# Performance work log

Hardware: AMD Instinct MI355X
Metric: run time of the kernel (lower is better)

The kernel has to match this reference:

```python
import jax, jax.numpy as jnp
import numpy as np

N = 50000      # nodes
E = 500000     # edges
D = 128        # model dim (in_dim == out_dim)
H = 8          # heads
DH = D // H    # head dim = 16
BN_EPS = 1e-5
Z_EPS = 1e-6


def setup_inputs() -> dict:
    key = jax.random.key(0)
    ks = jax.random.split(key, 24)
    w = lambda k, shape, s=0.05: (jax.random.normal(k, shape, jnp.float32) * s)
    inp = {}
    inp['v'] = jax.random.normal(ks[0], (N, D), jnp.float32)
    inp['e'] = jax.random.normal(ks[1], (E, D), jnp.float32)
    inp['envelope'] = jax.random.uniform(ks[2], (E, 1, 1), jnp.float32)
    inp['src'] = jax.random.randint(ks[3], (E,), 0, N, jnp.int32)
    inp['dst'] = jax.random.randint(ks[4], (E,), 0, N, jnp.int32)
    # attention projections (use_bias=False)
    inp['WQ'] = w(ks[5], (D, D)); inp['WK'] = w(ks[6], (D, D))
    inp['WV'] = w(ks[7], (D, D)); inp['We'] = w(ks[8], (D, D))
    # output projections
    inp['WO_v'] = w(ks[9], (D, D)); inp['bO_v'] = jnp.zeros((D,), jnp.float32)
    inp['WO_e'] = w(ks[10], (D, D)); inp['bO_e'] = jnp.zeros((D,), jnp.float32)
    # batch-norm affine params
    inp['g1_v'] = jnp.ones((D,), jnp.float32); inp['b1_v'] = jnp.zeros((D,), jnp.float32)
    inp['g1_e'] = jnp.ones((D,), jnp.float32); inp['b1_e'] = jnp.zeros((D,), jnp.float32)
    inp['g2_v'] = jnp.ones((D,), jnp.float32); inp['b2_v'] = jnp.zeros((D,), jnp.float32)
    inp['g2_e'] = jnp.ones((D,), jnp.float32); inp['b2_e'] = jnp.zeros((D,), jnp.float32)
    # FFN weights (hidden = 2*D)
    inp['W1v'] = w(ks[11], (D, 2 * D)); inp['b1v'] = jnp.zeros((2 * D,), jnp.float32)
    inp['W2v'] = w(ks[12], (2 * D, D)); inp['b2v'] = jnp.zeros((D,), jnp.float32)
    inp['W1e'] = w(ks[13], (D, 2 * D)); inp['b1e'] = jnp.zeros((2 * D,), jnp.float32)
    inp['W2e'] = w(ks[14], (2 * D, D)); inp['b2e'] = jnp.zeros((D,), jnp.float32)
    return inp


def _batchnorm(x, g, b):
    # BatchNorm1d in training mode: biased batch stats over axis 0
    m = x.mean(0)
    var = x.var(0)
    return (x - m) * jax.lax.rsqrt(var + BN_EPS) * g + b


def _forward(v, e, envelope, src, dst,
             WQ, WK, WV, We, WO_v, bO_v, WO_e, bO_e,
             g1_v, b1_v, g1_e, b1_e,
             W1v, b1v, W2v, b2v, W1e, b1e, W2e, b2e,
             g2_v, b2_v, g2_e, b2_e):
    # --- multi-head edge attention ---
    Q = (v @ WQ).reshape(N, H, DH)
    K = (v @ WK).reshape(N, H, DH)
    V = (v @ WV).reshape(N, H, DH)
    pe = (e @ We).reshape(E, H, DH)
    # score = K[src] * Q[dst] / sqrt(Dh) * proj_e   (elementwise, per head)
    score = K[src] * Q[dst] / np.sqrt(DH).astype(np.float32) * pe  # [E,H,Dh]
    e_attn = score.reshape(E, D)                                    # e_out
    s = jnp.exp(jnp.clip(score.sum(-1, keepdims=True), -5.0, 5.0))  # [E,H,1]
    msg = V[src] * envelope * s                                     # [E,H,Dh]
    wV = jax.ops.segment_sum(msg, dst, num_segments=N)              # [N,H,Dh]
    z = jax.ops.segment_sum(s, dst, num_segments=N)                 # [N,H,1]
    v_attn = (wV / (z + Z_EPS)).reshape(N, D)
    # --- O projection + residual + batchnorm ---
    v1 = _batchnorm(v + (v_attn @ WO_v + bO_v), g1_v, b1_v)
    e1 = _batchnorm(e + (e_attn @ WO_e + bO_e), g1_e, b1_e)
    # --- FFN + residual + batchnorm ---
    v2 = _batchnorm(v1 + (jax.nn.relu(v1 @ W1v + b1v) @ W2v + b2v), g2_v, b2_v)
    e2 = _batchnorm(e1 + (jax.nn.relu(e1 @ W1e + b1e) @ W2e + b2e), g2_e, b2_e)
    return v2, e2


def reference(v, e, envelope, src, dst,
              WQ, WK, WV, We, WO_v, bO_v, WO_e, bO_e,
              g1_v, b1_v, g1_e, b1_e,
              W1v, b1v, W2v, b2v, W1e, b1e, W2e, b2e,
              g2_v, b2_v, g2_e, b2_e):
    return _forward(v, e, envelope, src, dst,
                    WQ, WK, WV, We, WO_v, bO_v, WO_e, bO_e,
                    g1_v, b1_v, g1_e, b1_e,
                    W1v, b1v, W2v, b2v, W1e, b1e, W2e, b2e,
                    g2_v, b2_v, g2_e, b2_e)
```

## Files before the change

### kernel.cpp

```cpp
#include <hip/hip_runtime.h>
#include <hip/hip_bf16.h>

#define N_NODES 50000
#define N_EDGES 500000
#define DIM 128
#define RSTRIDE 256

typedef __bf16 bf16_t;
typedef __bf16 bf16x8 __attribute__((ext_vector_type(8)));
typedef __bf16 bf16x4 __attribute__((ext_vector_type(4)));
typedef __bf16 bf16x2 __attribute__((ext_vector_type(2)));
typedef float f32x4 __attribute__((ext_vector_type(4)));

#define MFMA(a,b,c) __builtin_amdgcn_mfma_f32_16x16x32_bf16((a),(b),(c),0,0,0)

__device__ __forceinline__ int swz(int row, int kbyte){ return kbyte ^ ((row & 7) << 4); }
__device__ __forceinline__ int hswz(int row, int kbyte){ return kbyte ^ ((row & 15) << 4); }

__device__ __forceinline__ bf16x8 lds_frag(const char* s, int row, int rowb, int kbyte){
  return *(const bf16x8*)(s + row * rowb + swz(row, kbyte));
}

__device__ __forceinline__ void copy16(char* dst, const char* __restrict__ src, int bytes){
  for (int o = threadIdx.x * 16; o < bytes; o += blockDim.x * 16)
    *(f32x4*)(dst + o) = *(const f32x4*)(src + o);
}

struct WPrep {
  const float* w[10];
  int Kd[10], Nd[10], off[10], cum[10], mode[10];
};

__global__ void k_wprep(WPrep d, char* img, int total){
  for (int idx = blockIdx.x * blockDim.x + threadIdx.x; idx < total; idx += gridDim.x * blockDim.x){
    int i = 0;
#pragma unroll
    for (int j = 1; j < 10; j++) if (idx >= d.cum[j]) i = j;
    int loc = idx - d.cum[i];
    int K = d.Kd[i], N = d.Nd[i];
    int n = loc / K, k = loc - n * K;
    float val = d.w[i][(size_t)k * N + n];
    int nn = n;
    if (d.mode[i] == 1) nn = ((n & 7) << 4) | (n >> 3);
    if (d.mode[i] == 4){ int w7 = n & 127; nn = ((n >> 7) << 7) | ((w7 & 7) << 4) | (w7 >> 3); }
    *(bf16_t*)(img + d.off[i] + nn * (K * 2) + swz(nn, k * 2)) = (bf16_t)val;
  }
}

__global__ void k_count(const int* __restrict__ dst, int* __restrict__ cnt){
  int i = blockIdx.x * blockDim.x + threadIdx.x;
  if (i < N_EDGES) atomicAdd(&cnt[dst[i]], 1);
}

__global__ __launch_bounds__(1024) void k_scan(const int* __restrict__ cnt,
                                               int* __restrict__ rowptr, int* __restrict__ wp){
  __shared__ int wsum[16];
  __shared__ int wpre[16];
  __shared__ int scarry;
  const int tid = threadIdx.x, lane = tid & 63, wv = tid >> 6;
  if (tid == 0) scarry = 0;
  for (int base = 0; base < N_NODES; base += 8192){
    int i0 = base + tid * 8;
    int v[8], p[8];
    int tsum = 0;
#pragma unroll
    for (int j = 0; j < 8; j++){
      int idx = i0 + j;
      v[j] = (idx < N_NODES) ? cnt[idx] : 0;
      p[j] = tsum; tsum += v[j];
    }
    int x = tsum;
#pragma unroll
    for (int off = 1; off < 64; off <<= 1){
      int t = __shfl_up(x, off);
      if (lane >= off) x += t;
    }
    if (lane == 63) wsum[wv] = x;
    __syncthreads();
    if (tid == 0){
      int run = scarry;
#pragma unroll
      for (int j = 0; j < 16; j++){ int t = wsum[j]; wpre[j] = run; run += t; }
      scarry = run;
    }
    __syncthreads();
    int texcl = wpre[wv] + x - tsum;
#pragma unroll
    for (int j = 0; j < 8; j++){
      int idx = i0 + j;
      if (idx < N_NODES){ rowptr[idx] = texcl + p[j]; wp[idx] = texcl + p[j]; }
    }
    __syncthreads();
  }
  if (tid == 0) rowptr[N_NODES] = scarry;
}

__global__ void k_fill(const int* __restrict__ dst, int* __restrict__ wp, int* __restrict__ csr){
  int i = blockIdx.x * blockDim.x + threadIdx.x;
  if (i < N_EDGES){
    int p = atomicAdd(&wp[dst[i]], 1);
    csr[p] = i;
  }
}

__global__ __launch_bounds__(512) void k_qkv(
    const float* __restrict__ v, const char* __restrict__ img,
    bf16_t* __restrict__ Q, bf16_t* __restrict__ K, bf16_t* __restrict__ V, int M)
{
  __shared__ __align__(16) char sm[65536];
  char* sX = sm;
  char* sW = sm + 32768;
  const int tid = threadIdx.x, lane = tid & 63, wave = tid >> 6;
  const int r0 = blockIdx.x * 128;
  for (int c = tid; c < 2048; c += 512){
    int row = c >> 4, kc = c & 15, grow = r0 + row;
    float f[8];
    if (grow < M){
      const float4* p = (const float4*)(v + (size_t)grow * DIM + kc * 8);
      float4 u0 = p[0], u1 = p[1];
      f[0]=u0.x; f[1]=u0.y; f[2]=u0.z; f[3]=u0.w;
      f[4]=u1.x; f[5]=u1.y; f[6]=u1.z; f[7]=u1.w;
    } else {
#pragma unroll
      for (int j=0;j<8;j++) f[j] = 0.f;
    }
    bf16x8 o;
#pragma unroll
    for (int j=0;j<8;j++) o[j] = (bf16_t)f[j];
    *(bf16x8*)(sX + row * 256 + swz(row, kc * 16)) = o;
  }
  const int rowA = wave * 16 + (lane & 15);
  const int kb0 = (lane >> 4) * 16;
  const int crow = wave*16 + (lane >> 4)*4;
  const int ccol = lane & 15;
  const f32x4 zero4 = {0.f, 0.f, 0.f, 0.f};
#pragma unroll
  for (int w3 = 0; w3 < 3; w3++){
    __syncthreads();
    copy16(sW, img + w3 * 32768, 32768);
    __syncthreads();
    f32x4 acc[8];
#pragma unroll
    for (int b=0;b<8;b++) acc[b] = zero4;
#pragma unroll
    for (int ks=0; ks<4; ks++){
      bf16x8 a = lds_frag(sX, rowA, 256, ks*64 + kb0);
#pragma unroll
      for (int nt=0; nt<8; nt++){
        int rn = nt*16 + (lane & 15);
        bf16x8 b = lds_frag(sW, rn, 256, ks*64 + kb0);
        acc[nt] = MFMA(a, b, acc[nt]);
      }
    }
    bf16_t* o = (w3 == 0) ? Q : ((w3 == 1) ? K : V);
#pragma unroll
    for (int r=0; r<4; r++){
      int grow = r0 + crow + r;
      if (grow < M){
        bf16x8 t;
#pragma unroll
        for (int nt=0; nt<8; nt++) t[nt] = (bf16_t)acc[nt][r];
        *(bf16x8*)(o + (size_t)grow * DIM + ccol*8) = t;
      }
    }
  }
}

__global__ __launch_bounds__(512, 4) void k_edge(
    const float* __restrict__ e,
    const int* __restrict__ src, const int* __restrict__ dst,
    const bf16_t* __restrict__ Qb, const bf16_t* __restrict__ Kb,
    const char* __restrict__ imgWe, const char* __restrict__ imgWo,
    const float* __restrict__ bOe,
    bf16_t* __restrict__ e1_pre, float* __restrict__ sv,
    float* __restrict__ stats, int M)
{
  __shared__ __align__(16) char sm[66560];
  char* sBuf = sm;
  char* sE   = sm + 32768;
  float* sStats = (float*)(sm + 65536);
  const int tid = threadIdx.x, lane = tid & 63, wave = tid >> 6;
  const int r0 = blockIdx.x * 128;
  const int q = lane >> 4, ccol = lane & 15;
  const int crow = wave*16 + q*4;
  const int rowA = wave*16 + ccol;
  const int kb0 = q * 16;
  bf16x8 Kg[4], Qg[4];
#pragma unroll
  for (int r=0;r<4;r++){
    int ed = r0 + crow + r; if (ed >= M) ed = M - 1;
    int sn = src[ed], dn = dst[ed];
    Kg[r] = *(const bf16x8*)(Kb + (size_t)sn * DIM + ccol * 8);
    Qg[r] = *(const bf16x8*)(Qb + (size_t)dn * DIM + ccol * 8);
  }
  int grA = r0 + rowA; if (grA >= M) grA = M - 1;
  const f32x4* epA = (const f32x4*)(e + (size_t)grA * DIM);
  f32x4 ea[8];
#pragma unroll
  for (int ks=0; ks<4; ks++){
    ea[2*ks]   = epA[ks*8 + q*2];
    ea[2*ks+1] = epA[ks*8 + q*2 + 1];
  }
  copy16(sBuf, imgWe, 32768);
  bf16x8 eAb[4];
#pragma unroll
  for (int ks=0; ks<4; ks++){
#pragma unroll
    for (int j=0;j<4;j++){
      eAb[ks][j]   = (bf16_t)ea[2*ks][j];
      eAb[ks][4+j] = (bf16_t)ea[2*ks+1][j];
    }
  }
#pragma unroll
  for (int ks=0; ks<4; ks++)
    *(bf16x8*)(sE + rowA*256 + swz(rowA, ks*64 + kb0)) = eAb[ks];
  __syncthreads();
  const f32x4 zero4 = {0.f,0.f,0.f,0.f};
  f32x4 pe[8];
#pragma unroll
  for (int i=0;i<8;i++) pe[i] = zero4;
#pragma unroll
  for (int ks=0; ks<4; ks++){
#pragma unroll
    for (int nt=0; nt<8; nt++){
      bf16x8 b = lds_frag(sBuf, nt*16 + ccol, 256, ks*64 + kb0);
      pe[nt] = MFMA(eAb[ks], b, pe[nt]);
    }
  }
  __syncthreads();
#pragma unroll
  for (int r=0;r<4;r++){
    int row = crow + r;
    bf16x8 t;
    float hsum = 0.f;
#pragma unroll
    for (int nt=0; nt<8; nt++){
      float sc = pe[nt][r] * 0.25f * (float)Kg[r][nt] * (float)Qg[r][nt];
      t[nt] = (bf16_t)sc;
      hsum += sc;
    }
    *(bf16x8*)(sBuf + row*256 + swz(row, ccol*16)) = t;
    float ts = hsum + __shfl_xor(hsum, 1);
    int ed = r0 + row;
    if (!(ccol & 1) && ed < M)
      sv[(size_t)ed*8 + (ccol >> 1)] = __expf(fminf(5.f, fmaxf(-5.f, ts)));
  }
  bf16x8 w2a[4];
#pragma unroll
  for (int ks=0; ks<4; ks++)
    w2a[ks] = *(const bf16x8*)(imgWo + rowA*256 + swz(rowA, ks*64 + kb0));
  __syncthreads();
  f32x4 a2[8];
#pragma unroll
  for (int i=0;i<8;i++) a2[i] = zero4;
#pragma unroll
  for (int ks=0; ks<4; ks++){
#pragma unroll
    for (int nt=0; nt<8; nt++){
      bf16x8 b = lds_frag(sBuf, nt*16 + ccol, 256, ks*64 + kb0);
      a2[nt] = MFMA(w2a[ks], b, a2[nt]);
    }
  }
  float4 bo = *(const float4*)(bOe + crow);
  float s1[4] = {0.f,0.f,0.f,0.f}, s2[4] = {0.f,0.f,0.f,0.f};
#pragma unroll
  for (int nt=0; nt<8; nt++){
    int m = nt*16 + ccol;
    int erow = r0 + m;
    bf16x4 u = *(const bf16x4*)(sE + m*256 + swz(m, crow*2));
    float val[4];
    val[0] = a2[nt][0] + (float)u[0] + bo.x;
    val[1] = a2[nt][1] + (float)u[1] + bo.y;
    val[2] = a2[nt][2] + (float)u[2] + bo.z;
    val[3] = a2[nt][3] + (float)u[3] + bo.w;
    if (erow < M){
      bf16x4 t;
#pragma unroll
      for (int r=0;r<4;r++) t[r] = (bf16_t)val[r];
      *(bf16x4*)(e1_pre + (size_t)erow*RSTRIDE + crow) = t;
    } else {
#pragma unroll
      for (int r=0;r<4;r++) val[r] = 0.f;
    }
#pragma unroll
    for (int r=0;r<4;r++){ s1[r] += val[r]; s2[r] += val[r]*val[r]; }
  }
#pragma unroll
  for (int r=0;r<4;r++){
    s1[r] += __shfl_xor(s1[r], 1); s1[r] += __shfl_xor(s1[r], 2);
    s1[r] += __shfl_xor(s1[r], 4); s1[r] += __shfl_xor(s1[r], 8);
    s2[r] += __shfl_xor(s2[r], 1); s2[r] += __shfl_xor(s2[r], 2);
    s2[r] += __shfl_xor(s2[r], 4); s2[r] += __shfl_xor(s2[r], 8);
  }
  if (ccol == 0){
#pragma unroll
    for (int r=0;r<4;r++){
      sStats[crow + r] = s1[r];
      sStats[128 + crow + r] = s2[r];
    }
  }
  __syncthreads();
  if (tid < 256) unsafeAtomicAdd(&stats[tid], sStats[tid]);
}

__global__ __launch_bounds__(512) void k_agg(
    const int* __restrict__ rowptr, const int* __restrict__ csr,
    const int* __restrict__ src, const float* __restrict__ envl,
    const float* __restrict__ sv, const bf16_t* __restrict__ V,
    bf16_t* __restrict__ vAttn, int M)
{
  const int wave = threadIdx.x >> 6, lane = threadIdx.x & 63;
  const int n = blockIdx.x * 8 + wave;
  if (n >= M) return;
  const int beg = rowptr[n], end = rowptr[n + 1];
  const int h = lane >> 3;
  float ax = 0.f, ay = 0.f, zacc = 0.f;
  int i = beg;
  for (; i + 4 <= end; i += 4){
    int e0 = csr[i], e1 = csr[i+1], e2 = csr[i+2], e3 = csr[i+3];
    int sn0 = src[e0], sn1 = src[e1], sn2 = src[e2], sn3 = src[e3];
    float sv0 = sv[(size_t)e0*8 + h], sv1 = sv[(size_t)e1*8 + h];
    float sv2 = sv[(size_t)e2*8 + h], sv3 = sv[(size_t)e3*8 + h];
    float n0 = envl[e0], n1 = envl[e1], n2 = envl[e2], n3 = envl[e3];
    bf16x2 a0 = *(const bf16x2*)(V + (size_t)sn0 * DIM + lane * 2);
    bf16x2 a1 = *(const bf16x2*)(V + (size_t)sn1 * DIM + lane * 2);
    bf16x2 a2v = *(const bf16x2*)(V + (size_t)sn2 * DIM + lane * 2);
    bf16x2 a3 = *(const bf16x2*)(V + (size_t)sn3 * DIM + lane * 2);
    float w0 = n0*sv0, w1 = n1*sv1, w2 = n2*sv2, w3 = n3*sv3;
    ax += (float)a0[0]*w0 + (float)a1[0]*w1 + (float)a2v[0]*w2 + (float)a3[0]*w3;
    ay += (float)a0[1]*w0 + (float)a1[1]*w1 + (float)a2v[1]*w2 + (float)a3[1]*w3;
    zacc += sv0 + sv1 + sv2 + sv3;
  }
  for (; i < end; i++){
    int eid = csr[i];
    int sn = src[eid];
    float s = sv[(size_t)eid * 8 + h];
    float env = envl[eid];
    const bf16x2 vv = *(const bf16x2*)(V + (size_t)sn * DIM + lane * 2);
    float w = env * s;
    ax += (float)vv[0] * w; ay += (float)vv[1] * w;
    zacc += s;
  }
  float inv = 1.f / (zacc + 1e-6f);
  bf16x2 o; o[0] = (bf16_t)(ax * inv); o[1] = (bf16_t)(ay * inv);
  *(bf16x2*)(vAttn + (size_t)n * DIM + lane * 2) = o;
}

__global__ __launch_bounds__(512) void k_nodeout(
    const bf16_t* __restrict__ vAttn, const float* __restrict__ v,
    const char* __restrict__ imgWo, const float* __restrict__ bOv,
    bf16_t* __restrict__ v1_pre, float* __restrict__ stats, int M)
{
  __shared__ __align__(16) char sm[66560];
  char* sW = sm;
  char* sX = sm + 32768;
  float* sStats = (float*)(sm + 65536);
  const int tid = threadIdx.x, lane = tid & 63, wave = tid >> 6;
  const int r0 = blockIdx.x * 128;
  copy16(sW, imgWo, 32768);
  if (tid < 256) sStats[tid] = 0.f;
  for (int c = tid; c < 2048; c += 512){
    int row = c >> 4, kc = c & 15, grow = r0 + row;
    bf16x8 o;
    if (grow < M){
      o = *(const bf16x8*)(vAttn + (size_t)grow * DIM + kc * 8);
    } else {
#pragma unroll
      for (int j=0;j<8;j++) o[j] = (bf16_t)0.f;
    }
    *(bf16x8*)(sX + row*256 + swz(row, kc*16)) = o;
  }
  __syncthreads();
  const int rowA = wave*16 + (lane & 15);
  const int kb0 = (lane >> 4)*16;
  const f32x4 zero4 = {0.f,0.f,0.f,0.f};
  f32x4 acc[8];
#pragma unroll
  for (int i=0;i<8;i++) acc[i]=zero4;
#pragma unroll
  for (int ks=0;ks<4;ks++){
    bf16x8 a = lds_frag(sX, rowA, 256, ks*64+kb0);
#pragma unroll
    for (int nt=0;nt<8;nt++){
      int rn = nt*16 + (lane&15);
      bf16x8 b = lds_frag(sW, rn, 256, ks*64+kb0);
      acc[nt] = MFMA(a,b,acc[nt]);
    }
  }
  const int crow = wave*16 + (lane>>4)*4;
  const int ccol = lane & 15;
  float4 bo0 = *(const float4*)(bOv + ccol*8);
  float4 bo1 = *(const float4*)(bOv + ccol*8 + 4);
  float s1[8], s2[8];
#pragma unroll
  for (int j=0;j<8;j++){ s1[j]=0.f; s2[j]=0.f; }
#pragma unroll
  for (int r=0;r<4;r++){
    int grow = r0 + crow + r;
    float val[8];
    if (grow < M){
      const float4* vp = (const float4*)(v + (size_t)grow*DIM + ccol*8);
      float4 v0 = vp[0], v1 = vp[1];
      val[0]=acc[0][r]+v0.x+bo0.x; val[1]=acc[1][r]+v0.y+bo0.y;
      val[2]=acc[2][r]+v0.z+bo0.z; val[3]=acc[3][r]+v0.w+bo0.w;
      val[4]=acc[4][r]+v1.x+bo1.x; val[5]=acc[5][r]+v1.y+bo1.y;
      val[6]=acc[6][r]+v1.z+bo1.z; val[7]=acc[7][r]+v1.w+bo1.w;
      bf16x8 t;
#pragma unroll
      for (int j=0;j<8;j++) t[j] = (bf16_t)val[j];
      *(bf16x8*)(v1_pre + (size_t)grow*RSTRIDE + ccol*8) = t;
    } else {
#pragma unroll
      for (int j=0;j<8;j++) val[j]=0.f;
    }
#pragma unroll
    for (int j=0;j<8;j++){ s1[j] += val[j]; s2[j] += val[j]*val[j]; }
  }
#pragma unroll
  for (int j=0;j<8;j++){
    s1[j] += __shfl_xor(s1[j], 16); s1[j] += __shfl_xor(s1[j], 32);
    s2[j] += __shfl_xor(s2[j], 16); s2[j] += __shfl_xor(s2[j], 32);
  }
  if (lane < 16){
#pragma unroll
    for (int j=0;j<8;j++){
      atomicAdd(&sStats[ccol*8 + j], s1[j]);
      atomicAdd(&sStats[128 + ccol*8 + j], s2[j]);
    }
  }
  __syncthreads();
  if (tid < 256) unsafeAtomicAdd(&stats[tid], sStats[tid]);
}

struct FinArgs { const float* st; const float* g; const float* b; float* ss; float invM; };

__global__ void k_finstats(FinArgs a0, FinArgs a1){
  FinArgs a = (blockIdx.x == 0) ? a0 : a1;
  int c = threadIdx.x;
  float mean = a.st[c] * a.invM;
  float var  = a.st[128 + c] * a.invM - mean * mean;
  float scl  = a.g[c] * rsqrtf(var + 1e-5f);
  a.ss[c] = scl;
  a.ss[128 + c] = a.b[c] - mean * scl;
}

__global__ __launch_bounds__(512, 4) void k_ffn(
    bf16_t* __restrict__ xio, const float* __restrict__ ss1,
    const char* __restrict__ img1, const float* __restrict__ b1,
    const char* __restrict__ img2, const float* __restrict__ b2,
    float* __restrict__ stats2, int M)
{
  __shared__ __align__(16) char sm[66560];
  char* sA = sm;
  char* sB = sm + 32768;
  float* sStats = (float*)(sm + 65536);
  const int tid = threadIdx.x, lane = tid & 63, wave = tid >> 6;
  const int r0 = blockIdx.x * 128;
  const int q = lane >> 4, ccol = lane & 15;
  const int kb0 = q * 16;
  const int crow = wave*16 + q*4;
  const int rowA = wave*16 + ccol;
  const f32x4 zero4 = {0.f,0.f,0.f,0.f};

  copy16(sB, img1, 32768);
  if (tid < 256) sStats[tid] = 0.f;
  int grA = r0 + rowA; if (grA >= M) grA = M - 1;
  const bf16_t* xrow = xio + (size_t)grA * RSTRIDE;
  bf16x8 araw[4];
#pragma unroll
  for (int ks=0; ks<4; ks++)
    araw[ks] = *(const bf16x8*)(xrow + ks*32 + q*8);
  bf16x8 xAb[4];
#pragma unroll
  for (int ks=0; ks<4; ks++){
    const f32x4* sp = (const f32x4*)(ss1 + ks*32 + q*8);
    const f32x4* hp = (const f32x4*)(ss1 + 128 + ks*32 + q*8);
    f32x4 s0 = sp[0], s1v = sp[1], h0 = hp[0], h1 = hp[1];
#pragma unroll
    for (int j=0;j<4;j++){
      xAb[ks][j]   = (bf16_t)((float)araw[ks][j]  *s0[j]  + h0[j]);
      xAb[ks][4+j] = (bf16_t)((float)araw[ks][4+j]*s1v[j] + h1[j]);
    }
  }
  __syncthreads();

  bf16x8 hreg0[4], hreg1[4];
  f32x4 wbuf[4];
#pragma unroll
  for (int i=0;i<4;i++) wbuf[i] = *(const f32x4*)(img1 + 32768 + tid*16 + i*8192);
  {
    float4 bq0 = *(const float4*)(b1 + ccol*8);
    float4 bq1 = *(const float4*)(b1 + ccol*8 + 4);
    f32x4 acc[8];
#pragma unroll
    for (int i=0;i<8;i++) acc[i]=zero4;
#pragma unroll
    for (int ks=0;ks<4;ks++){
#pragma unroll
      for (int nt=0;nt<8;nt++){
        bf16x8 b = lds_frag(sB, nt*16 + ccol, 256, ks*64+kb0);
        acc[nt] = MFMA(xAb[ks], b, acc[nt]);
      }
    }
#pragma unroll
    for (int r=0;r<4;r++){
      bf16x8 t;
      t[0]=(bf16_t)fmaxf(acc[0][r]+bq0.x,0.f); t[1]=(bf16_t)fmaxf(acc[1][r]+bq0.y,0.f);
      t[2]=(bf16_t)fmaxf(acc[2][r]+bq0.z,0.f); t[3]=(bf16_t)fmaxf(acc[3][r]+bq0.w,0.f);
      t[4]=(bf16_t)fmaxf(acc[4][r]+bq1.x,0.f); t[5]=(bf16_t)fmaxf(acc[5][r]+bq1.y,0.f);
      t[6]=(bf16_t)fmaxf(acc[6][r]+bq1.z,0.f); t[7]=(bf16_t)fmaxf(acc[7][r]+bq1.w,0.f);
      hreg0[r] = t;
    }
  }
  __syncthreads();
#pragma unroll
  for (int i=0;i<4;i++) *(f32x4*)(sB + tid*16 + i*8192) = wbuf[i];
#pragma unroll
  for (int r=0;r<4;r++){
    int row = crow + r;
    *(bf16x8*)(sA + row*256 + hswz(row, ccol*16)) = hreg0[r];
  }
  __syncthreads();

  f32x4 o2[8];
#pragma unroll
  for (int i=0;i<8;i++) o2[i]=zero4;
  {
    float4 bq2 = *(const float4*)(b1 + 128 + ccol*8);
    float4 bq3 = *(const float4*)(b1 + 128 + ccol*8 + 4);
    f32x4 acc[8];
#pragma unroll
    for (int i=0;i<8;i++) acc[i]=zero4;
#pragma unroll
    for (int ks=0;ks<4;ks++){
#pragma unroll
      for (int nt=0;nt<8;nt++){
        bf16x8 b = lds_frag(sB, nt*16 + ccol, 256, ks*64+kb0);
        acc[nt] = MFMA(xAb[ks], b, acc[nt]);
      }
    }
#pragma unroll
    for (int r=0;r<4;r++){
      bf16x8 t;
      t[0]=(bf16_t)fmaxf(acc[0][r]+bq2.x,0.f); t[1]=(bf16_t)fmaxf(acc[1][r]+bq2.y,0.f);
      t[2]=(bf16_t)fmaxf(acc[2][r]+bq2.z,0.f); t[3]=(bf16_t)fmaxf(acc[3][r]+bq2.w,0.f);
      t[4]=(bf16_t)fmaxf(acc[4][r]+bq3.x,0.f); t[5]=(bf16_t)fmaxf(acc[5][r]+bq3.y,0.f);
      t[6]=(bf16_t)fmaxf(acc[6][r]+bq3.z,0.f); t[7]=(bf16_t)fmaxf(acc[7][r]+bq3.w,0.f);
      hreg1[r] = t;
    }
  }
  {
    bf16x8 w2a[4];
#pragma unroll
    for (int ks=0; ks<4; ks++)
      w2a[ks] = *(const bf16x8*)(img2 + (size_t)rowA*512 + swz(rowA, ks*64 + kb0));
#pragma unroll
    for (int ks=0; ks<4; ks++){
#pragma unroll
      for (int nt=0; nt<8; nt++){
        int m = nt*16 + ccol;
        bf16x8 b = *(const bf16x8*)(sA + m*256 + hswz(m, ks*64 + kb0));
        o2[nt] = MFMA(w2a[ks], b, o2[nt]);
      }
    }
  }
  __syncthreads();
#pragma unroll
  for (int r=0;r<4;r++){
    int row = crow + r;
    *(bf16x8*)(sA + row*256 + hswz(row, ccol*16)) = hreg1[r];
  }
  __syncthreads();
  {
    bf16x8 w2a[4];
#pragma unroll
    for (int ks=0; ks<4; ks++)
      w2a[ks] = *(const bf16x8*)(img2 + (size_t)rowA*512 + swz(rowA, 256 + ks*64 + kb0));
#pragma unroll
    for (int ks=0; ks<4; ks++){
#pragma unroll
      for (int nt=0; nt<8; nt++){
        int m = nt*16 + ccol;
        bf16x8 b = *(const bf16x8*)(sA + m*256 + hswz(m, ks*64 + kb0));
        o2[nt] = MFMA(w2a[ks], b, o2[nt]);
      }
    }
  }
#pragma unroll
  for (int nt=0; nt<8; nt++){
    int m = nt*16 + ccol;
    bf16x4 t;
#pragma unroll
    for (int r=0;r<4;r++) t[r] = (bf16_t)o2[nt][r];
    *(bf16x4*)(sB + m*256 + swz(m, crow*2)) = t;
  }
  __syncthreads();

  float4 sc0 = *(const float4*)(ss1 + ccol*8);
  float4 sc1 = *(const float4*)(ss1 + ccol*8 + 4);
  float4 sh0 = *(const float4*)(ss1 + 128 + ccol*8);
  float4 sh1 = *(const float4*)(ss1 + 128 + ccol*8 + 4);
  float4 b20 = *(const float4*)(b2 + ccol*8);
  float4 b21 = *(const float4*)(b2 + ccol*8 + 4);
  float s1[8], s2[8];
#pragma unroll
  for (int j=0;j<8;j++){ s1[j]=0.f; s2[j]=0.f; }
#pragma unroll
  for (int r=0;r<4;r++){
    int row = crow + r, grow = r0 + row;
    float val[8];
    if (grow < M){
      bf16x8 u = *(const bf16x8*)(xio + (size_t)grow*RSTRIDE + ccol*8);
      bf16x8 ob = *(const bf16x8*)(sB + row*256 + swz(row, ccol*16));
      val[0]=(float)u[0]*sc0.x+sh0.x + (float)ob[0]+b20.x;
      val[1]=(float)u[1]*sc0.y+sh0.y + (float)ob[1]+b20.y;
      val[2]=(float)u[2]*sc0.z+sh0.z + (float)ob[2]+b20.z;
      val[3]=(float)u[3]*sc0.w+sh0.w + (float)ob[3]+b20.w;
      val[4]=(float)u[4]*sc1.x+sh1.x + (float)ob[4]+b21.x;
      val[5]=(float)u[5]*sc1.y+sh1.y + (float)ob[5]+b21.y;
      val[6]=(float)u[6]*sc1.z+sh1.z + (float)ob[6]+b21.z;
      val[7]=(float)u[7]*sc1.w+sh1.w + (float)ob[7]+b21.w;
      bf16x8 t;
#pragma unroll
      for (int j=0;j<8;j++) t[j] = (bf16_t)val[j];
      *(bf16x8*)(xio + (size_t)grow*RSTRIDE + ccol*8) = t;
    } else {
#pragma unroll
      for (int j=0;j<8;j++) val[j]=0.f;
    }
#pragma unroll
    for (int j=0;j<8;j++){ s1[j] += val[j]; s2[j] += val[j]*val[j]; }
  }
#pragma unroll
  for (int j=0;j<8;j++){
    s1[j] += __shfl_xor(s1[j], 16); s1[j] += __shfl_xor(s1[j], 32);
    s2[j] += __shfl_xor(s2[j], 16); s2[j] += __shfl_xor(s2[j], 32);
  }
  if (lane < 16){
#pragma unroll
    for (int j=0;j<8;j++){
      atomicAdd(&sStats[ccol*8 + j], s1[j]);
      atomicAdd(&sStats[128 + ccol*8 + j], s2[j]);
    }
  }
  __syncthreads();
  if (tid < 256) unsafeAtomicAdd(&stats2[tid], sStats[tid]);
}

struct NormP { const float* st; const float* g; const float* bn; float invM; };

__global__ __launch_bounds__(256) void k_norm2(
    char* __restrict__ xv, char* __restrict__ xe,
    NormP pv, NormP pe, long long nv, long long ne)
{
  __shared__ float sSS[512];
  const int tid = threadIdx.x;
  {
    int side = tid >> 7, c = tid & 127;
    NormP pp = side ? pe : pv;
    float mean = pp.st[c] * pp.invM;
    float var  = pp.st[128 + c] * pp.invM - mean * mean;
    float scl  = pp.g[c] * rsqrtf(var + 1e-5f);
    sSS[side*256 + c] = scl;
    sSS[side*256 + 128 + c] = pp.bn[c] - mean * scl;
  }
  __syncthreads();
  long long tv = nv * 16, total = tv + ne * 16;
  for (long long g = (long long)blockIdx.x * blockDim.x + tid; g < total;
       g += (long long)gridDim.x * blockDim.x){
    bool isv = g < tv;
    char* base = isv ? xv : xe;
    const float* ss = isv ? sSS : (sSS + 256);
    long long gg = isv ? g : g - tv;
    long long row = gg >> 4;
    int c = (int)(gg & 15);
    bf16x8 u = *(const bf16x8*)(base + row * 512 + c * 16);
    int c0 = c * 8;
    float4 o0, o1;
    o0.x = (float)u[0]*ss[c0+0] + ss[128+c0+0];
    o0.y = (float)u[1]*ss[c0+1] + ss[128+c0+1];
    o0.z = (float)u[2]*ss[c0+2] + ss[128+c0+2];
    o0.w = (float)u[3]*ss[c0+3] + ss[128+c0+3];
    o1.x = (float)u[4]*ss[c0+4] + ss[128+c0+4];
    o1.y = (float)u[5]*ss[c0+5] + ss[128+c0+5];
    o1.z = (float)u[6]*ss[c0+6] + ss[128+c0+6];
    o1.w = (float)u[7]*ss[c0+7] + ss[128+c0+7];
    float4* dp = (float4*)(base + row * 512 + c * 32);
    dp[0] = o0; dp[1] = o1;
  }
}

extern "C" void kernel_launch(void* const* d_in, const int* in_sizes, int n_in,
                              void* d_out, int out_size, void* d_ws, size_t ws_size,
                              hipStream_t stream)
{
  const float* v    = (const float*)d_in[0];
  const float* e    = (const float*)d_in[1];
  const float* envl = (const float*)d_in[2];
  const int*   src  = (const int*)d_in[3];
  const int*   dst  = (const int*)d_in[4];
  const float* bOv  = (const float*)d_in[10];
  const float* bOe  = (const float*)d_in[12];
  const float* g1v  = (const float*)d_in[13];
  const float* b1vn = (const float*)d_in[14];
  const float* g1e  = (const float*)d_in[15];
  const float* b1en = (const float*)d_in[16];
  const float* g2v  = (const float*)d_in[17];
  const float* b2vn = (const float*)d_in[18];
  const float* g2e  = (const float*)d_in[19];
  const float* b2en = (const float*)d_in[20];
  const float* b1vf = (const float*)d_in[22];
  const float* b2vf = (const float*)d_in[24];
  const float* b1ef = (const float*)d_in[26];
  const float* b2ef = (const float*)d_in[28];

  float* out_v = (float*)d_out;
  float* out_e = out_v + (size_t)N_NODES * DIM;
  bf16_t* v1b = (bf16_t*)out_v;
  bf16_t* e1b = (bf16_t*)out_e;

  char* ws = (char*)d_ws;
  const size_t IMG_OFF = 0;
  const size_t QB_OFF  = 458752;
  const size_t KB_OFF  = QB_OFF  + 12800000;
  const size_t VB_OFF  = KB_OFF  + 12800000;
  const size_t VA_OFF  = VB_OFF  + 12800000;
  const size_t SV_OFF  = VA_OFF  + 12800000;
  const size_t CSR_OFF = SV_OFF  + 16000000;
  const size_t RP_OFF  = CSR_OFF + 2000000;
  const size_t WP_OFF  = RP_OFF  + 200016;
  const size_t CNT_OFF = WP_OFF  + 200000;
  const size_t ST_OFF  = CNT_OFF + 200000;
  const size_t SS_OFF  = ST_OFF  + 4096;

  char*   img   = ws + IMG_OFF;
  bf16_t* Qb    = (bf16_t*)(ws + QB_OFF);
  bf16_t* Kb    = (bf16_t*)(ws + KB_OFF);
  bf16_t* Vb    = (bf16_t*)(ws + VB_OFF);
  bf16_t* vAttn = (bf16_t*)(ws + VA_OFF);
  float*  svp   = (float*)(ws + SV_OFF);
  int*    csr   = (int*)(ws + CSR_OFF);
  int*    rowp  = (int*)(ws + RP_OFF);
  int*    wpp   = (int*)(ws + WP_OFF);
  int*    cnt   = (int*)(ws + CNT_OFF);
  float*  st    = (float*)(ws + ST_OFF);
  float*  ssb   = (float*)(ws + SS_OFF);
  float* st_e1 = st;        float* st_v1 = st + 256;
  float* st_v2 = st + 512;  float* st_e2 = st + 768;
  float* ss_v1 = ssb;       float* ss_e1 = ssb + 256;

  (void)hipMemsetAsync(ws + CNT_OFF, 0, 200000 + 4096, stream);

  WPrep wp;
  const int wid[10]   = {5,6,7,8,9,11,21,23,25,27};
  const int Ks[10]    = {128,128,128,128,128,128,128,256,128,256};
  const int Ns[10]    = {128,128,128,128,128,128,256,128,256,128};
  const int modes[10] = {1,1,1,1,1,0,4,0,4,0};
  int cum = 0, off = 0;
  for (int i = 0; i < 10; i++){
    wp.w[i] = (const float*)d_in[wid[i]];
    wp.Kd[i] = Ks[i]; wp.Nd[i] = Ns[i];
    wp.off[i] = off; wp.cum[i] = cum; wp.mode[i] = modes[i];
    off += Ks[i]*Ns[i]*2; cum += Ks[i]*Ns[i];
  }
  k_wprep<<<896, 256, 0, stream>>>(wp, img, cum);

  k_count<<<1954, 256, 0, stream>>>(dst, cnt);
  k_scan<<<1, 1024, 0, stream>>>(cnt, rowp, wpp);
  k_fill<<<1954, 256, 0, stream>>>(dst, wpp, csr);

  k_qkv<<<391, 512, 0, stream>>>(v, img, Qb, Kb, Vb, N_NODES);

  k_edge<<<3907, 512, 0, stream>>>(e, src, dst, Qb, Kb,
                                   img + 98304 , img + 163840 , bOe,
                                   e1b, svp, st_e1, N_EDGES);

  k_agg<<<6250, 512, 0, stream>>>(rowp, csr, src, envl, svp, Vb, vAttn, N_NODES);

  k_nodeout<<<391, 512, 0, stream>>>(vAttn, v, img + 131072 , bOv,
                                     v1b, st_v1, N_NODES);

  {
    FinArgs fv{st_v1, g1v, b1vn, ss_v1, 1.f / N_NODES};
    FinArgs fe{st_e1, g1e, b1en, ss_e1, 1.f / N_EDGES};
    k_finstats<<<2, 128, 0, stream>>>(fv, fe);
  }

  k_ffn<<<391, 512, 0, stream>>>(v1b, ss_v1, img + 196608 , b1vf,
                                 img + 262144 , b2vf, st_v2, N_NODES);
  k_ffn<<<3907, 512, 0, stream>>>(e1b, ss_e1, img + 327680 , b1ef,
                                  img + 393216 , b2ef, st_e2, N_EDGES);

  NormP npv{st_v2, g2v, b2vn, 1.f / N_NODES};
  NormP npe{st_e2, g2e, b2en, 1.f / N_EDGES};
  k_norm2<<<4096, 256, 0, stream>>>((char*)out_v, (char*)out_e, npv, npe,
                                    (long long)N_NODES, (long long)N_EDGES);
}
```

Before: 617.7 us.

## Process two 128-edge tiles per k_edge block with prefetch of second tile

Each k_edge block now handles two consecutive 128-edge tiles, so the grid halves. The Wo weight fragments and bias load once per block, and the per-block stats atomics are issued half as often. The second tile's e rows are loaded into registers while the first tile's output projection runs, overlapping global loads with MFMA work. The cost is higher register pressure from holding eaB, which may reduce occupancy under launch_bounds(512,4), and the We image is still copied into LDS again for the second tile.

```diff
diff --git a/kernel.cpp b/kernel.cpp
--- a/kernel.cpp
+++ b/kernel.cpp
@@ -180,110 +180,216 @@
   char* sE   = sm + 32768;
   float* sStats = (float*)(sm + 65536);
   const int tid = threadIdx.x, lane = tid & 63, wave = tid >> 6;
-  const int r0 = blockIdx.x * 128;
+  const int r0A = blockIdx.x * 256;
+  const int r0B = r0A + 128;
   const int q = lane >> 4, ccol = lane & 15;
   const int crow = wave*16 + q*4;
   const int rowA = wave*16 + ccol;
   const int kb0 = q * 16;
+  const f32x4 zero4 = {0.f,0.f,0.f,0.f};
+  const float4 bo = *(const float4*)(bOe + crow);
+  float s1[4] = {0.f,0.f,0.f,0.f}, s2[4] = {0.f,0.f,0.f,0.f};
+
   bf16x8 Kg[4], Qg[4];
 #pragma unroll
   for (int r=0;r<4;r++){
-    int ed = r0 + crow + r; if (ed >= M) ed = M - 1;
+    int ed = r0A + crow + r; if (ed >= M) ed = M - 1;
     int sn = src[ed], dn = dst[ed];
     Kg[r] = *(const bf16x8*)(Kb + (size_t)sn * DIM + ccol * 8);
     Qg[r] = *(const bf16x8*)(Qb + (size_t)dn * DIM + ccol * 8);
   }
-  int grA = r0 + rowA; if (grA >= M) grA = M - 1;
-  const f32x4* epA = (const f32x4*)(e + (size_t)grA * DIM);
-  f32x4 ea[8];
-#pragma unroll
-  for (int ks=0; ks<4; ks++){
-    ea[2*ks]   = epA[ks*8 + q*2];
-    ea[2*ks+1] = epA[ks*8 + q*2 + 1];
-  }
-  copy16(sBuf, imgWe, 32768);
-  bf16x8 eAb[4];
-#pragma unroll
-  for (int ks=0; ks<4; ks++){
-#pragma unroll
-    for (int j=0;j<4;j++){
-      eAb[ks][j]   = (bf16_t)ea[2*ks][j];
-      eAb[ks][4+j] = (bf16_t)ea[2*ks+1][j];
-    }
-  }
-#pragma unroll
-  for (int ks=0; ks<4; ks++)
-    *(bf16x8*)(sE + rowA*256 + swz(rowA, ks*64 + kb0)) = eAb[ks];
-  __syncthreads();
-  const f32x4 zero4 = {0.f,0.f,0.f,0.f};
-  f32x4 pe[8];
-#pragma unroll
-  for (int i=0;i<8;i++) pe[i] = zero4;
-#pragma unroll
-  for (int ks=0; ks<4; ks++){
-#pragma unroll
-    for (int nt=0; nt<8; nt++){
-      bf16x8 b = lds_frag(sBuf, nt*16 + ccol, 256, ks*64 + kb0);
-      pe[nt] = MFMA(eAb[ks], b, pe[nt]);
-    }
-  }
-  __syncthreads();
-#pragma unroll
-  for (int r=0;r<4;r++){
-    int row = crow + r;
-    bf16x8 t;
-    float hsum = 0.f;
-#pragma unroll
-    for (int nt=0; nt<8; nt++){
-      float sc = pe[nt][r] * 0.25f * (float)Kg[r][nt] * (float)Qg[r][nt];
-      t[nt] = (bf16_t)sc;
-      hsum += sc;
-    }
-    *(bf16x8*)(sBuf + row*256 + swz(row, ccol*16)) = t;
-    float ts = hsum + __shfl_xor(hsum, 1);
-    int ed = r0 + row;
-    if (!(ccol & 1) && ed < M)
-      sv[(size_t)ed*8 + (ccol >> 1)] = __expf(fminf(5.f, fmaxf(-5.f, ts)));
+  int grA = r0A + rowA; if (grA >= M) grA = M - 1;
+  {
+    const f32x4* epA = (const f32x4*)(e + (size_t)grA * DIM);
+    f32x4 ea[8];
+#pragma unroll
+    for (int ks=0; ks<4; ks++){
+      ea[2*ks]   = epA[ks*8 + q*2];
+      ea[2*ks+1] = epA[ks*8 + q*2 + 1];
+    }
+    copy16(sBuf, imgWe, 32768);
+    bf16x8 eAb[4];
+#pragma unroll
+    for (int ks=0; ks<4; ks++){
+#pragma unroll
+      for (int j=0;j<4;j++){
+        eAb[ks][j]   = (bf16_t)ea[2*ks][j];
+        eAb[ks][4+j] = (bf16_t)ea[2*ks+1][j];
+      }
+    }
+#pragma unroll
+    for (int ks=0; ks<4; ks++)
+      *(bf16x8*)(sE + rowA*256 + swz(rowA, ks*64 + kb0)) = eAb[ks];
+    __syncthreads();
+    f32x4 pe[8];
+#pragma unroll
+    for (int i=0;i<8;i++) pe[i] = zero4;
+#pragma unroll
+    for (int ks=0; ks<4; ks++){
+#pragma unroll
+      for (int nt=0; nt<8; nt++){
+        bf16x8 b = lds_frag(sBuf, nt*16 + ccol, 256, ks*64 + kb0);
+        pe[nt] = MFMA(eAb[ks], b, pe[nt]);
+      }
+    }
+    __syncthreads();
+#pragma unroll
+    for (int r=0;r<4;r++){
+      int row = crow + r;
+      bf16x8 t;
+      float hsum = 0.f;
+#pragma unroll
+      for (int nt=0; nt<8; nt++){
+        float sc = pe[nt][r] * 0.25f * (float)Kg[r][nt] * (float)Qg[r][nt];
+        t[nt] = (bf16_t)sc;
+        hsum += sc;
+      }
+      *(bf16x8*)(sBuf + row*256 + swz(row, ccol*16)) = t;
+      float ts = hsum + __shfl_xor(hsum, 1);
+      int ed = r0A + row;
+      if (!(ccol & 1) && ed < M)
+        sv[(size_t)ed*8 + (ccol >> 1)] = __expf(fminf(5.f, fmaxf(-5.f, ts)));
+    }
+  }
+  int grB = r0B + rowA; if (grB >= M) grB = M - 1;
+  f32x4 eaB[8];
+  {
+    const f32x4* epB = (const f32x4*)(e + (size_t)grB * DIM);
+#pragma unroll
+    for (int ks=0; ks<4; ks++){
+      eaB[2*ks]   = epB[ks*8 + q*2];
+      eaB[2*ks+1] = epB[ks*8 + q*2 + 1];
+    }
   }
   bf16x8 w2a[4];
 #pragma unroll
   for (int ks=0; ks<4; ks++)
     w2a[ks] = *(const bf16x8*)(imgWo + rowA*256 + swz(rowA, ks*64 + kb0));
   __syncthreads();
-  f32x4 a2[8];
-#pragma unroll
-  for (int i=0;i<8;i++) a2[i] = zero4;
-#pragma unroll
-  for (int ks=0; ks<4; ks++){
+  {
+    f32x4 a2[8];
+#pragma unroll
+    for (int i=0;i<8;i++) a2[i] = zero4;
+#pragma unroll
+    for (int ks=0; ks<4; ks++){
+#pragma unroll
+      for (int nt=0; nt<8; nt++){
+        bf16x8 b = lds_frag(sBuf, nt*16 + ccol, 256, ks*64 + kb0);
+        a2[nt] = MFMA(w2a[ks], b, a2[nt]);
+      }
+    }
 #pragma unroll
     for (int nt=0; nt<8; nt++){
-      bf16x8 b = lds_frag(sBuf, nt*16 + ccol, 256, ks*64 + kb0);
-      a2[nt] = MFMA(w2a[ks], b, a2[nt]);
-    }
-  }
-  float4 bo = *(const float4*)(bOe + crow);
-  float s1[4] = {0.f,0.f,0.f,0.f}, s2[4] = {0.f,0.f,0.f,0.f};
-#pragma unroll
-  for (int nt=0; nt<8; nt++){
-    int m = nt*16 + ccol;
-    int erow = r0 + m;
-    bf16x4 u = *(const bf16x4*)(sE + m*256 + swz(m, crow*2));
-    float val[4];
-    val[0] = a2[nt][0] + (float)u[0] + bo.x;
-    val[1] = a2[nt][1] + (float)u[1] + bo.y;
-    val[2] = a2[nt][2] + (float)u[2] + bo.z;
-    val[3] = a2[nt][3] + (float)u[3] + bo.w;
-    if (erow < M){
-      bf16x4 t;
-#pragma unroll
-      for (int r=0;r<4;r++) t[r] = (bf16_t)val[r];
-      *(bf16x4*)(e1_pre + (size_t)erow*RSTRIDE + crow) = t;
-    } else {
-#pragma unroll
-      for (int r=0;r<4;r++) val[r] = 0.f;
-    }
-#pragma unroll
-    for (int r=0;r<4;r++){ s1[r] += val[r]; s2[r] += val[r]*val[r]; }
+      int m = nt*16 + ccol;
+      int erow = r0A + m;
+      bf16x4 u = *(const bf16x4*)(sE + m*256 + swz(m, crow*2));
+      float val[4];
+      val[0] = a2[nt][0] + (float)u[0] + bo.x;
+      val[1] = a2[nt][1] + (float)u[1] + bo.y;
+      val[2] = a2[nt][2] + (float)u[2] + bo.z;
+      val[3] = a2[nt][3] + (float)u[3] + bo.w;
+      if (erow < M){
+        bf16x4 t;
+#pragma unroll
+        for (int r=0;r<4;r++) t[r] = (bf16_t)val[r];
+        *(bf16x4*)(e1_pre + (size_t)erow*RSTRIDE + crow) = t;
+      } else {
+#pragma unroll
+        for (int r=0;r<4;r++) val[r] = 0.f;
+      }
+#pragma unroll
+      for (int r=0;r<4;r++){ s1[r] += val[r]; s2[r] += val[r]*val[r]; }
+    }
+  }
+  __syncthreads();
+
+#pragma unroll
+  for (int r=0;r<4;r++){
+    int ed = r0B + crow + r; if (ed >= M) ed = M - 1;
+    int sn = src[ed], dn = dst[ed];
+    Kg[r] = *(const bf16x8*)(Kb + (size_t)sn * DIM + ccol * 8);
+    Qg[r] = *(const bf16x8*)(Qb + (size_t)dn * DIM + ccol * 8);
+  }
+  copy16(sBuf, imgWe, 32768);
+  {
+    bf16x8 eAb[4];
+#pragma unroll
+    for (int ks=0; ks<4; ks++){
+#pragma unroll
+      for (int j=0;j<4;j++){
+        eAb[ks][j]   = (bf16_t)eaB[2*ks][j];
+        eAb[ks][4+j] = (bf16_t)eaB[2*ks+1][j];
+      }
+    }
+#pragma unroll
+    for (int ks=0; ks<4; ks++)
+      *(bf16x8*)(sE + rowA*256 + swz(rowA, ks*64 + kb0)) = eAb[ks];
+    __syncthreads();
+    f32x4 pe[8];
+#pragma unroll
+    for (int i=0;i<8;i++) pe[i] = zero4;
+#pragma unroll
+    for (int ks=0; ks<4; ks++){
+#pragma unroll
+      for (int nt=0; nt<8; nt++){
+        bf16x8 b = lds_frag(sBuf, nt*16 + ccol, 256, ks*64 + kb0);
+        pe[nt] = MFMA(eAb[ks], b, pe[nt]);
+      }
+    }
+    __syncthreads();
+#pragma unroll
+    for (int r=0;r<4;r++){
+      int row = crow + r;
+      bf16x8 t;
+      float hsum = 0.f;
+#pragma unroll
+      for (int nt=0; nt<8; nt++){
+        float sc = pe[nt][r] * 0.25f * (float)Kg[r][nt] * (float)Qg[r][nt];
+        t[nt] = (bf16_t)sc;
+        hsum += sc;
+      }
+      *(bf16x8*)(sBuf + row*256 + swz(row, ccol*16)) = t;
+      float ts = hsum + __shfl_xor(hsum, 1);
+      int ed = r0B + row;
+      if (!(ccol & 1) && ed < M)
+        sv[(size_t)ed*8 + (ccol >> 1)] = __expf(fminf(5.f, fmaxf(-5.f, ts)));
+    }
+  }
+  __syncthreads();
+  {
+    f32x4 a2[8];
+#pragma unroll
+    for (int i=0;i<8;i++) a2[i] = zero4;
+#pragma unroll
+    for (int ks=0; ks<4; ks++){
+#pragma unroll
+      for (int nt=0; nt<8; nt++){
+        bf16x8 b = lds_frag(sBuf, nt*16 + ccol, 256, ks*64 + kb0);
+        a2[nt] = MFMA(w2a[ks], b, a2[nt]);
+      }
+    }
+#pragma unroll
+    for (int nt=0; nt<8; nt++){
+      int m = nt*16 + ccol;
+      int erow = r0B + m;
+      bf16x4 u = *(const bf16x4*)(sE + m*256 + swz(m, crow*2));
+      float val[4];
+      val[0] = a2[nt][0] + (float)u[0] + bo.x;
+      val[1] = a2[nt][1] + (float)u[1] + bo.y;
+      val[2] = a2[nt][2] + (float)u[2] + bo.z;
+      val[3] = a2[nt][3] + (float)u[3] + bo.w;
+      if (erow < M){
+        bf16x4 t;
+#pragma unroll
+        for (int r=0;r<4;r++) t[r] = (bf16_t)val[r];
+        *(bf16x4*)(e1_pre + (size_t)erow*RSTRIDE + crow) = t;
+      } else {
+#pragma unroll
+        for (int r=0;r<4;r++) val[r] = 0.f;
+      }
+#pragma unroll
+      for (int r=0;r<4;r++){ s1[r] += val[r]; s2[r] += val[r]*val[r]; }
+    }
   }
 #pragma unroll
   for (int r=0;r<4;r++){
@@ -771,7 +877,7 @@
 
   k_qkv<<<391, 512, 0, stream>>>(v, img, Qb, Kb, Vb, N_NODES);
 
-  k_edge<<<3907, 512, 0, stream>>>(e, src, dst, Qb, Kb,
+  k_edge<<<1954, 512, 0, stream>>>(e, src, dst, Qb, Kb,
                                    img + 98304 , img + 163840 , bOe,
                                    e1b, svp, st_e1, N_EDGES);
 
```

Result: slower. 727.8 us (+17.8%).
